# Kernel tuning notes

Measured on AMD Instinct MI355X. Metric: run time of the kernel, lower is better.

## Reference

```python
import jax, jax.numpy as jnp
import numpy as np

NEG_INF = -1e9


def setup_inputs() -> dict:
    key = jax.random.key(0)
    ks = jax.random.split(key, 12)
    B, Tq, Tki, E, D, M = 4, 2048, 2048, 1024, 128, 16384
    return {
        "x": jax.random.normal(ks[0], (B, Tq, E), jnp.float32),
        "ki": jax.random.normal(ks[1], (B, Tki, E), jnp.float32),
        "vi": jax.random.normal(ks[2], (B, Tki, E), jnp.float32),
        "mem_keys": jax.random.normal(ks[3], (B, M, D), jnp.float32),
        "mem_vals": jax.random.normal(ks[4], (B, M, D), jnp.float32),
        "Wq": jax.random.normal(ks[5], (E, D), jnp.float32) / np.sqrt(E),
        "bq": jax.random.normal(ks[6], (D,), jnp.float32) * 0.02,
        "Wk": jax.random.normal(ks[7], (E, D), jnp.float32) / np.sqrt(E),
        "bk": jax.random.normal(ks[8], (D,), jnp.float32) * 0.02,
        "Wv": jax.random.normal(ks[9], (E, D), jnp.float32) / np.sqrt(E),
        "bv": jax.random.normal(ks[10], (D,), jnp.float32) * 0.02,
        "gate": jax.random.normal(ks[11], (1,), jnp.float32),
        "idx": 3,
    }


def reference(x, ki, vi, mem_keys, mem_vals, Wq, bq, Wk, bk, Wv, bv, gate, idx):
    B, Tq, E = x.shape
    D = Wq.shape[1]
    top_k = 32
    q = x @ Wq + bq            # [B,Tq,D]
    k = x @ Wk + bk            # [B,Tq,D]
    v = x @ Wv + bv
    s = idx * D                # idx is a python int -> static slice
    k_full = jnp.concatenate([ki[:, :, s:s + D], k], axis=1)   # [B,Tk,D]
    v_full = jnp.concatenate([vi[:, :, s:s + D], v], axis=1)
    Tk = k_full.shape[1]
    # causal SDPA over prefix+current, offset diagonal Tk-Tq
    scores = jnp.einsum("bqd,bkd->bqk", q, k_full) / jnp.sqrt(jnp.float32(D))
    i = jnp.arange(Tq)[:, None]
    j = jnp.arange(Tk)[None, :]
    causal = j <= i + (Tk - Tq)
    scores = jnp.where(causal, scores, NEG_INF)
    att = jax.nn.softmax(scores, axis=-1)
    out = jnp.einsum("bqk,bkd->bqd", att, v_full)              # [B,Tq,D]
    # kNN memory attention: exact top-k inner-product search per query
    mem_scores = jnp.einsum("btd,bmd->btm", q, mem_keys)       # [B,Tq,M]
    _, top_idx = jax.lax.top_k(mem_scores, top_k)              # [B,Tq,K]
    gather = jax.vmap(lambda mem, ix: mem[ix])                 # per batch
    mem_k = gather(mem_keys, top_idx)                          # [B,Tq,K,D]
    mem_v = gather(mem_vals, top_idx)
    # note: original scales by sqrt(Cq)=sqrt(n_embd), not sqrt(head_size)
    mem_att = jax.nn.softmax(
        jnp.einsum("btd,btkd->btk", q, mem_k) / jnp.sqrt(jnp.float32(E)), axis=-1)
    mem_out = jnp.einsum("btk,btkd->btd", mem_att, mem_v)      # [B,Tq,D]
    md_out = out * gate + mem_out * (1.0 - gate)
    return md_out
```

## Files before the change

### kernel.cpp

```cpp
#include <hip/hip_runtime.h>


using bf16x8 = __attribute__((ext_vector_type(8))) short;
using f32x4  = __attribute__((ext_vector_type(4))) float;

typedef __attribute__((address_space(1))) const void GVoid;
typedef __attribute__((address_space(3))) void LVoid;
__device__ __forceinline__ void gl16(const ushort* g, ushort* l) {
  __builtin_amdgcn_global_load_lds((GVoid*)g, (LVoid*)l, 16, 0, 0);
}

__device__ __forceinline__ float bf2f(ushort h) {
  union { uint u; float f; } x; x.u = ((uint)h) << 16; return x.f;
}
__device__ __forceinline__ ushort f2bf(float f) {
  union { float f; uint u; } x; x.f = f;
  uint u = x.u;
  u += 0x7fffu + ((u >> 16) & 1u);
  return (ushort)(u >> 16);
}
__device__ __forceinline__ uint ord2(uint v) {
  uint s = (v >> 15) & 0x00010001u;
  uint t = (s << 15) - s;
  return v ^ t ^ 0x80008000u;
}

__global__ __launch_bounds__(256) void k_wt(const float* __restrict__ Wq,
                                            const float* __restrict__ Wk,
                                            const float* __restrict__ Wv,
                                            ushort* __restrict__ Wth,
                                            ushort* __restrict__ Wtlq) {
  int id = blockIdx.x * 256 + threadIdx.x;
  int z = id >> 17, r = id & 131071;
  int n = r >> 10, k = r & 1023;
  const float* W = (z == 1) ? Wk : (z == 2) ? Wv : Wq;
  float w = W[k * 128 + n];
  ushort h = f2bf(w);
  if (z < 3) Wth[id] = h;
  else       Wtlq[r] = f2bf(w - bf2f(h));
}

__global__ __launch_bounds__(256) void k_cvt8(const float* __restrict__ src,
                                              ushort* __restrict__ dst) {
  int id = blockIdx.x * 256 + threadIdx.x;
  size_t base = (size_t)id * 8;
  float4 a = *(const float4*)(src + base);
  float4 b = *(const float4*)(src + base + 4);
  bf16x8 r;
  r[0] = (short)f2bf(a.x); r[1] = (short)f2bf(a.y);
  r[2] = (short)f2bf(a.z); r[3] = (short)f2bf(a.w);
  r[4] = (short)f2bf(b.x); r[5] = (short)f2bf(b.y);
  r[6] = (short)f2bf(b.z); r[7] = (short)f2bf(b.w);
  *(bf16x8*)(dst + base) = r;
}

__global__ __launch_bounds__(256) void k_xsplit(const float* __restrict__ x,
                                                ushort* __restrict__ xh,
                                                ushort* __restrict__ xl) {
  int id = blockIdx.x * 256 + threadIdx.x;
  size_t base = (size_t)id * 8;
  float4 a = *(const float4*)(x + base);
  float4 b = *(const float4*)(x + base + 4);
  float xf[8] = {a.x, a.y, a.z, a.w, b.x, b.y, b.z, b.w};
  bf16x8 rh, rl;
#pragma unroll
  for (int j = 0; j < 8; ++j) {
    ushort h = f2bf(xf[j]);
    rh[j] = (short)h;
    rl[j] = (short)f2bf(xf[j] - bf2f(h));
  }
  *(bf16x8*)(xh + base) = rh;
  *(bf16x8*)(xl + base) = rl;
}

__global__ __launch_bounds__(256) void k_prefix(const float* __restrict__ ki,
                                                const float* __restrict__ vi,
                                                const int* __restrict__ idx,
                                                ushort* __restrict__ kfull,
                                                ushort* __restrict__ vfull) {
  int s = idx[0] * 128;
  int id = blockIdx.x * 256 + threadIdx.x;
  int d8 = (id & 15) * 8;
  int bt = id >> 4;
  int b = bt >> 11, t = bt & 2047;
  const float* kp = ki + (size_t)bt * 1024 + s + d8;
  const float* vp = vi + (size_t)bt * 1024 + s + d8;
  bf16x8 rk, rv;
#pragma unroll
  for (int j = 0; j < 8; ++j) { rk[j] = (short)f2bf(kp[j]); rv[j] = (short)f2bf(vp[j]); }
  size_t dst = ((size_t)b * 4096 + t) * 128 + d8;
  *(bf16x8*)(kfull + dst) = rk;
  *(bf16x8*)(vfull + dst) = rv;
}

__global__ __launch_bounds__(256) void k_qkv3(const ushort* __restrict__ xh,
                                              const ushort* __restrict__ xl,
                                              const ushort* __restrict__ Wth,
                                              const ushort* __restrict__ Wtlq,
                                              const float* __restrict__ bq,
                                              const float* __restrict__ bk,
                                              const float* __restrict__ bv,
                                              float* __restrict__ qex,
                                              ushort* __restrict__ kfull,
                                              ushort* __restrict__ vfull) {
  __shared__ ushort lds[2][16384];
  int z = blockIdx.z;
  int g = blockIdx.y;
  int m0 = blockIdx.x * 64;
  int tid = threadIdx.x;
  int w = tid >> 6, lane = tid & 63;
  int l15 = lane & 15, q8 = (lane >> 4) * 8;
  const ushort* Wz = Wth + (size_t)z * 131072;
  const ushort* xh_src = xh + (size_t)(m0 + w * 16 + l15) * 1024 + q8;
  const ushort* xl_src = xl + (size_t)(m0 + w * 16 + l15) * 1024 + q8;
  const ushort* wh_src = Wz   + (size_t)(g * 64 + w * 16 + l15) * 1024 + q8;
  const ushort* wl_src = Wtlq + (size_t)(g * 64 + w * 16 + l15) * 1024 + q8;
  int sb = w * 1024;

  f32x4 zero = {0.f, 0.f, 0.f, 0.f};
  f32x4 acc[4] = {zero, zero, zero, zero};

  {
    ushort* B = &lds[0][0];
    gl16(xh_src,      B + sb);
    gl16(xh_src + 32, B + sb + 512);
    gl16(wh_src,      B + 8192 + sb);
    gl16(wh_src + 32, B + 8192 + sb + 512);
    if (z == 0) {
      gl16(xl_src,      B + 4096 + sb);
      gl16(xl_src + 32, B + 4096 + sb + 512);
      gl16(wl_src,      B + 12288 + sb);
      gl16(wl_src + 32, B + 12288 + sb + 512);
    }
  }
  __syncthreads();
  int bf = 0;
  for (int t16 = 0; t16 < 16; ++t16) {
    if (t16 < 15) {
      int k0 = t16 * 64 + 64;
      ushort* B = &lds[bf ^ 1][0];
      gl16(xh_src + k0,      B + sb);
      gl16(xh_src + k0 + 32, B + sb + 512);
      gl16(wh_src + k0,      B + 8192 + sb);
      gl16(wh_src + k0 + 32, B + 8192 + sb + 512);
      if (z == 0) {
        gl16(xl_src + k0,      B + 4096 + sb);
        gl16(xl_src + k0 + 32, B + 4096 + sb + 512);
        gl16(wl_src + k0,      B + 12288 + sb);
        gl16(wl_src + k0 + 32, B + 12288 + sb + 512);
      }
    }
    const ushort* B = &lds[bf][0];
    int lo = lane * 8;
    if (z == 0) {
#pragma unroll
      for (int kc = 0; kc < 2; ++kc) {
        bf16x8 ah = *(const bf16x8*)(B + (w * 2 + kc) * 512 + lo);
        bf16x8 al = *(const bf16x8*)(B + 4096 + (w * 2 + kc) * 512 + lo);
#pragma unroll
        for (int cc = 0; cc < 4; ++cc) {
          bf16x8 bh = *(const bf16x8*)(B + 8192 + (cc * 2 + kc) * 512 + lo);
          bf16x8 bl = *(const bf16x8*)(B + 12288 + (cc * 2 + kc) * 512 + lo);
          acc[cc] = __builtin_amdgcn_mfma_f32_16x16x32_bf16(ah, bh, acc[cc], 0, 0, 0);
          acc[cc] = __builtin_amdgcn_mfma_f32_16x16x32_bf16(ah, bl, acc[cc], 0, 0, 0);
          acc[cc] = __builtin_amdgcn_mfma_f32_16x16x32_bf16(al, bh, acc[cc], 0, 0, 0);
        }
      }
    } else {
#pragma unroll
      for (int kc = 0; kc < 2; ++kc) {
        bf16x8 ah = *(const bf16x8*)(B + (w * 2 + kc) * 512 + lo);
#pragma unroll
        for (int cc = 0; cc < 4; ++cc) {
          bf16x8 bh = *(const bf16x8*)(B + 8192 + (cc * 2 + kc) * 512 + lo);
          acc[cc] = __builtin_amdgcn_mfma_f32_16x16x32_bf16(ah, bh, acc[cc], 0, 0, 0);
        }
      }
    }
    __syncthreads();
    bf ^= 1;
  }

  const float* bias = (z == 0) ? bq : (z == 1) ? bk : bv;
  int mrow = m0 + w * 16 + (lane >> 4) * 4;
#pragma unroll
  for (int cc = 0; cc < 4; ++cc) {
    int n = g * 64 + cc * 16 + l15;
    float bb = bias[n];
#pragma unroll
    for (int r = 0; r < 4; ++r) {
      int m = mrow + r;
      float val = acc[cc][r] + bb;
      if (z == 0) {
        qex[(size_t)m * 128 + n] = val;
      } else {
        int b2 = m >> 11, tt = m & 2047;
        size_t o = ((size_t)b2 * 4096 + 2048 + tt) * 128 + n;
        if (z == 1) kfull[o] = f2bf(val); else vfull[o] = f2bf(val);
      }
    }
  }
}

__global__ __launch_bounds__(256) void k_vt(const ushort* __restrict__ vfull,
                                            ushort* __restrict__ Vt) {
  __shared__ ushort lds[64][136];
  int blk = blockIdx.x;
  int b = blk >> 6, t0 = (blk & 63) * 64;
  int t = threadIdx.x;
#pragma unroll
  for (int p = 0; p < 4; ++p) {
    int ch = p * 256 + t;
    int row = ch >> 4, c8 = (ch & 15) * 8;
    uint4 v = *(const uint4*)(vfull + ((size_t)b * 4096 + t0 + row) * 128 + c8);
    *(uint4*)(&lds[row][c8]) = v;
  }
  __syncthreads();
#pragma unroll
  for (int p = 0; p < 8; ++p) {
    int q = p * 256 + t;
    int d = q >> 4, t4 = (q & 15) * 4;
    ushort4 o;
    o.x = lds[t4 + 0][d]; o.y = lds[t4 + 1][d];
    o.z = lds[t4 + 2][d]; o.w = lds[t4 + 3][d];
    *(ushort4*)(Vt + ((size_t)b * 128 + d) * 4096 + t0 + t4) = o;
  }
}

__global__ __launch_bounds__(256) void k_scores(const float* __restrict__ A,
                                                const ushort* __restrict__ Bm,
                                                ushort* __restrict__ S,
                                                int N, int nslice, int causalOff,
                                                long sA, long sB, long sS) {
  __shared__ ushort Bt[64 * 136];
  int q0 = blockIdx.x * 64;
  int ns0 = blockIdx.y * nslice;
  int nend = ns0 + nslice; if (nend > N) nend = N;
  int climit = q0 + 64 + causalOff; if (nend > climit) nend = climit;
  if (ns0 >= nend) return;
  int zb = blockIdx.z;
  const float*  Ab = A  + (size_t)zb * sA;
  const ushort* Bb = Bm + (size_t)zb * sB;
  ushort* Sb = S + (size_t)zb * sS;
  int t = threadIdx.x, lane = t & 63, wv = t >> 6;
  int l15 = lane & 15, q8 = (lane >> 4) * 8;
  const float* Arow = Ab + (size_t)(q0 + wv * 16 + l15) * 128 + q8;
  bf16x8 af[4];
#pragma unroll
  for (int kc = 0; kc < 4; ++kc)
#pragma unroll
    for (int j = 0; j < 8; ++j) af[kc][j] = (short)f2bf(Arow[kc * 32 + j]);
  for (int n0 = ns0; n0 < nend; n0 += 64) {
#pragma unroll
    for (int p = 0; p < 4; ++p) {
      int ch = p * 256 + t;
      int row = ch >> 4, c8 = (ch & 15) * 8;
      uint4 v = *(const uint4*)(Bb + (size_t)(n0 + row) * 128 + c8);
      *(uint4*)(&Bt[row * 136 + c8]) = v;
    }
    __syncthreads();
    f32x4 zero = {0.f, 0.f, 0.f, 0.f};
    f32x4 acc[4] = {zero, zero, zero, zero};
#pragma unroll
    for (int h = 0; h < 4; ++h) {
#pragma unroll
      for (int kc = 0; kc < 4; ++kc) {
        bf16x8 bfr = *(const bf16x8*)(&Bt[(h * 16 + l15) * 136 + kc * 32 + q8]);
        acc[h] = __builtin_amdgcn_mfma_f32_16x16x32_bf16(af[kc], bfr, acc[h], 0, 0, 0);
      }
    }
    int qq = q0 + wv * 16 + (lane >> 4) * 4;
#pragma unroll
    for (int h = 0; h < 4; ++h)
#pragma unroll
      for (int r = 0; r < 4; ++r)
        Sb[(size_t)(qq + r) * N + (n0 + h * 16 + l15)] = f2bf(acc[h][r]);
    __syncthreads();
  }
}

__global__ __launch_bounds__(256) void k_softmax(ushort* __restrict__ S) {
  int rid = blockIdx.x;
  int i = rid & 2047;
  ushort* row = S + (size_t)rid * 4096;
  int w = i + 2049;
  int t = threadIdx.x;
  const float scale = 0.08838834764831845f;
  float v[16];
  float mx = -1e30f;
#pragma unroll
  for (int c = 0; c < 16; ++c) {
    int e = c * 256 + t;
    float f = -1e30f;
    if (e < w) f = bf2f(row[e]) * scale;
    v[c] = f;
    mx = fmaxf(mx, f);
  }
  __shared__ float red[4];
#pragma unroll
  for (int off = 32; off; off >>= 1) mx = fmaxf(mx, __shfl_xor(mx, off));
  if ((t & 63) == 0) red[t >> 6] = mx;
  __syncthreads();
  mx = fmaxf(fmaxf(red[0], red[1]), fmaxf(red[2], red[3]));
  __syncthreads();
  float ex[16];
  float sum = 0.f;
#pragma unroll
  for (int c = 0; c < 16; ++c) {
    int e = c * 256 + t;
    ex[c] = (e < w) ? __expf(v[c] - mx) : 0.f;
    sum += ex[c];
  }
#pragma unroll
  for (int off = 32; off; off >>= 1) sum += __shfl_xor(sum, off);
  if ((t & 63) == 0) red[t >> 6] = sum;
  __syncthreads();
  sum = red[0] + red[1] + red[2] + red[3];
  float inv = 1.f / sum;
#pragma unroll
  for (int c = 0; c < 16; ++c) {
    int e = c * 256 + t;
    row[e] = f2bf(ex[c] * inv);
  }
}

__global__ __launch_bounds__(128) void k_pv(const ushort* __restrict__ P,
                                            const ushort* __restrict__ Vt,
                                            float* __restrict__ O) {
  __shared__ ushort lds[2][4096];
  int b = blockIdx.z;
  int d0 = blockIdx.y * 32;
  int q0 = blockIdx.x * 32;
  int t = threadIdx.x, lane = t & 63, w = t >> 6;
  int l15 = lane & 15, q8 = (lane >> 4) * 8;
  const ushort* Pq = P + ((size_t)b * 2048 + q0) * 4096;
  const ushort* Vb = Vt + (size_t)b * 128 * 4096;
  const ushort* p_src = Pq + (size_t)(w * 16 + l15) * 4096 + q8;
  const ushort* v_src = Vb + (size_t)(d0 + w * 16 + l15) * 4096 + q8;
  int kend = q0 + 32 + 2048; if (kend > 4096) kend = 4096;
  int ksteps = (kend + 63) >> 6;

  f32x4 zero = {0.f, 0.f, 0.f, 0.f};
  f32x4 acc[2] = {zero, zero};

  {
    ushort* B = &lds[0][0];
    gl16(p_src,      B + (w * 2 + 0) * 512);
    gl16(p_src + 32, B + (w * 2 + 1) * 512);
    gl16(v_src,      B + 2048 + (w * 2 + 0) * 512);
    gl16(v_src + 32, B + 2048 + (w * 2 + 1) * 512);
  }
  __syncthreads();
  int bf = 0;
  for (int st = 0; st < ksteps; ++st) {
    if (st + 1 < ksteps) {
      int k0 = st * 64 + 64;
      ushort* B = &lds[bf ^ 1][0];
      gl16(p_src + k0,      B + (w * 2 + 0) * 512);
      gl16(p_src + k0 + 32, B + (w * 2 + 1) * 512);
      gl16(v_src + k0,      B + 2048 + (w * 2 + 0) * 512);
      gl16(v_src + k0 + 32, B + 2048 + (w * 2 + 1) * 512);
    }
    const ushort* B = &lds[bf][0];
    int lo = lane * 8;
#pragma unroll
    for (int kc = 0; kc < 2; ++kc) {
      bf16x8 af = *(const bf16x8*)(B + (w * 2 + kc) * 512 + lo);
#pragma unroll
      for (int nc = 0; nc < 2; ++nc) {
        bf16x8 bfr = *(const bf16x8*)(B + 2048 + (nc * 2 + kc) * 512 + lo);
        acc[nc] = __builtin_amdgcn_mfma_f32_16x16x32_bf16(af, bfr, acc[nc], 0, 0, 0);
      }
    }
    __syncthreads();
    bf ^= 1;
  }

  size_t ob = ((size_t)b * 2048 + q0 + w * 16 + (lane >> 4) * 4) * 128;
#pragma unroll
  for (int nc = 0; nc < 2; ++nc)
#pragma unroll
    for (int r = 0; r < 4; ++r)
      O[ob + (size_t)r * 128 + d0 + nc * 16 + l15] = acc[nc][r];
}

__global__ __launch_bounds__(256) void k_topk(const ushort* __restrict__ Sall,
                                              const float* __restrict__ qf32b,
                                              const float* __restrict__ memk,
                                              const float* __restrict__ memv,
                                              float* __restrict__ mout) {
  __shared__ uint sred[32];
  __shared__ float qf[128];
  __shared__ uint cidx[384];
  __shared__ float csc[384];
  __shared__ unsigned long long ckey[384];
  __shared__ uint selIdx[32];
  __shared__ float selS[32];
  __shared__ float obuf[256];
  __shared__ int nC;

  int i = blockIdx.x;
  const ushort* Srow = Sall + (size_t)i * 16384;
  int t = threadIdx.x;
  int wv = t >> 6, lane = t & 63;
  if (t < 128) qf[t] = qf32b[(size_t)i * 128 + t];
  if (t == 0) nC = 0;

  uint keys[32];
#pragma unroll
  for (int c = 0; c < 8; ++c) {
    int base = (c * 256 + t) * 8;
    uint4 rv = *(const uint4*)(Srow + base);
    keys[c * 4 + 0] = ord2(rv.x);
    keys[c * 4 + 1] = ord2(rv.y);
    keys[c * 4 + 2] = ord2(rv.z);
    keys[c * 4 + 3] = ord2(rv.w);
  }
  uint mymax = 0;
#pragma unroll
  for (int r = 0; r < 32; ++r) {
    uint v = keys[r];
    uint hi = v >> 16, lo = v & 0xffffu;
    uint mm = hi > lo ? hi : lo;
    mymax = mm > mymax ? mm : mymax;
  }
#pragma unroll
  for (int off = 32; off; off >>= 1) {
    uint o = __shfl_xor(mymax, off);
    mymax = o > mymax ? o : mymax;
  }
  if (lane == 0) sred[wv] = mymax;
  __syncthreads();
  uint M = sred[0];
  { uint a = sred[1]; M = a > M ? a : M;
    a = sred[2]; M = a > M ? a : M;
    a = sred[3]; M = a > M ? a : M; }
  __syncthreads();

  uint T;
  uint MbCur = M >> 5;
  uint carry = 0;
  while (true) {
    uint h0 = 0, h1 = 0;
#pragma unroll
    for (int r = 0; r < 32; ++r) {
      uint v = keys[r];
      uint blo = MbCur - ((v & 0xffffu) >> 5);
      uint bhi = MbCur - (v >> 21);
      if (blo < 8u) { uint a = 1u << ((blo & 3u) << 3); if (blo < 4u) h0 += a; else h1 += a; }
      if (bhi < 8u) { uint a = 1u << ((bhi & 3u) << 3); if (bhi < 4u) h0 += a; else h1 += a; }
    }
    uint c8[8] = {h0 & 255u, (h0 >> 8) & 255u, (h0 >> 16) & 255u, h0 >> 24,
                  h1 & 255u, (h1 >> 8) & 255u, (h1 >> 16) & 255u, h1 >> 24};
#pragma unroll
    for (int b = 0; b < 8; ++b)
#pragma unroll
      for (int off = 32; off; off >>= 1) c8[b] += __shfl_xor(c8[b], off);
    if (lane == 0) {
#pragma unroll
      for (int b = 0; b < 8; ++b) sred[wv * 8 + b] = c8[b];
    }
    __syncthreads();
    uint cum = carry; int bstar = -1;
#pragma unroll
    for (int b = 0; b < 8; ++b) {
      uint tb = sred[b] + sred[8 + b] + sred[16 + b] + sred[24 + b];
      cum += tb;
      if (bstar < 0 && cum >= 64u) bstar = b;
    }
    if (bstar >= 0) { T = (MbCur - (uint)bstar) << 5; break; }
    carry = cum;
    MbCur -= 8u;
    __syncthreads();
  }

#pragma unroll
  for (int r = 0; r < 32; ++r) {
    uint v = keys[r];
    int base = ((r >> 2) * 256 + t) * 8 + ((r & 3) * 2);
    if ((v & 0xffffu) >= T) { int p = atomicAdd(&nC, 1); if (p < 384) cidx[p] = (uint)base; }
    if ((v >> 16) >= T)     { int p = atomicAdd(&nC, 1); if (p < 384) cidx[p] = (uint)(base + 1); }
  }
  __syncthreads();
  int C = nC; if (C > 384) C = 384;
  {
    float qa = qf[lane * 2], qb = qf[lane * 2 + 1];
    for (int j0 = wv; j0 < C; j0 += 32) {
      float2 pp[8];
      float s[8];
#pragma unroll
      for (int u = 0; u < 8; ++u) {
        int j = j0 + u * 4;
        if (j < C) pp[u] = *(const float2*)(memk + (size_t)cidx[j] * 128 + lane * 2);
      }
#pragma unroll
      for (int u = 0; u < 8; ++u) {
        int j = j0 + u * 4;
        s[u] = (j < C) ? (qa * pp[u].x + qb * pp[u].y) : 0.f;
      }
#pragma unroll
      for (int off = 32; off; off >>= 1) {
#pragma unroll
        for (int u = 0; u < 8; ++u) s[u] += __shfl_xor(s[u], off);
      }
      if (lane == 0) {
#pragma unroll
        for (int u = 0; u < 8; ++u) {
          int j = j0 + u * 4;
          if (j < C) csc[j] = s[u];
        }
      }
    }
  }
  __syncthreads();
  for (int j = t; j < C; j += 256) {
    uint sb2 = __float_as_uint(csc[j]);
    uint o = (sb2 & 0x80000000u) ? ~sb2 : (sb2 | 0x80000000u);
    ckey[j] = ((unsigned long long)o << 32) | (uint)(~cidx[j]);
  }
  __syncthreads();
  for (int j = t; j < C; j += 256) {
    unsigned long long my = ckey[j];
    int rank = 0;
    for (int l = 0; l < C; ++l) rank += (ckey[l] > my) ? 1 : 0;
    if (rank < 32) { selS[rank] = csc[j]; selIdx[rank] = cidx[j]; }
  }
  __syncthreads();
  if (wv == 0) {
    float sc = (lane < 32) ? selS[lane] * 0.03125f : -1e30f;
    float mx = sc;
#pragma unroll
    for (int off = 32; off; off >>= 1) mx = fmaxf(mx, __shfl_xor(mx, off));
    float ex = (lane < 32) ? __expf(sc - mx) : 0.f;
    float Z = ex;
#pragma unroll
    for (int off = 32; off; off >>= 1) Z += __shfl_xor(Z, off);
    if (lane < 32) selS[lane] = ex / Z;
  }
  __syncthreads();
  {
    int d = t & 127, half = t >> 7;
    float vv[16];
#pragma unroll
    for (int u = 0; u < 16; ++u)
      vv[u] = memv[(size_t)selIdx[half * 16 + u] * 128 + d];
    float acc = 0.f;
#pragma unroll
    for (int u = 0; u < 16; ++u)
      acc += selS[half * 16 + u] * vv[u];
    obuf[t] = acc;
  }
  __syncthreads();
  if (t < 128) mout[(size_t)i * 128 + t] = obuf[t] + obuf[t + 128];
}

__global__ __launch_bounds__(256) void k_mix(const float* __restrict__ a,
                                             const float* __restrict__ b,
                                             const float* __restrict__ gate,
                                             float* __restrict__ out) {
  int id = blockIdx.x * 256 + threadIdx.x;
  float g = gate[0];
  float4 va = ((const float4*)a)[id];
  float4 vb = ((const float4*)b)[id];
  float4 o;
  o.x = va.x * g + vb.x * (1.f - g);
  o.y = va.y * g + vb.y * (1.f - g);
  o.z = va.z * g + vb.z * (1.f - g);
  o.w = va.w * g + vb.w * (1.f - g);
  ((float4*)out)[id] = o;
}

extern "C" void kernel_launch(void* const* d_in, const int* in_sizes, int n_in,
                              void* d_out, int out_size, void* d_ws, size_t ws_size,
                              hipStream_t stream) {
  const float* x    = (const float*)d_in[0];
  const float* ki   = (const float*)d_in[1];
  const float* vi   = (const float*)d_in[2];
  const float* mk   = (const float*)d_in[3];
  const float* mv   = (const float*)d_in[4];
  const float* Wq   = (const float*)d_in[5];
  const float* bq   = (const float*)d_in[6];
  const float* Wk   = (const float*)d_in[7];
  const float* bk   = (const float*)d_in[8];
  const float* Wv   = (const float*)d_in[9];
  const float* bv   = (const float*)d_in[10];
  const float* gate = (const float*)d_in[11];
  const int*   idx  = (const int*)d_in[12];

  char* ws = (char*)d_ws;
  ushort* Sbuf  = (ushort*)(ws);
  ushort* xh    = (ushort*)(ws);
  ushort* xl    = (ushort*)(ws + 16777216);
  float*  qex   = (float*) (ws + 67108864);
  ushort* kfull = (ushort*)(ws + 71303168);
  ushort* vfull = (ushort*)(ws + 75497472);
  ushort* Vt    = (ushort*)(ws + 79691776);
  ushort* mkb   = (ushort*)(ws + 83886080);
  ushort* Wth   = (ushort*)(ws + 100663296);
  ushort* Wtlq  = (ushort*)(ws + 101449728);
  float*  osdpa = (float*) (ws + 101711872);
  float*  mout  = (float*) (ws + 105906176);

  k_wt<<<2048, 256, 0, stream>>>(Wq, Wk, Wv, Wth, Wtlq);
  k_cvt8<<<4096, 256, 0, stream>>>(mk, mkb);
  k_xsplit<<<4096, 256, 0, stream>>>(x, xh, xl);
  k_prefix<<<512, 256, 0, stream>>>(ki, vi, idx, kfull, vfull);

  k_qkv3<<<dim3(128, 2, 3), 256, 0, stream>>>(xh, xl, Wth, Wtlq, bq, bk, bv,
                                              qex, kfull, vfull);
  k_vt<<<256, 256, 0, stream>>>(vfull, Vt);

  k_scores<<<dim3(32, 8, 4), 256, 0, stream>>>(qex, kfull, Sbuf,
                                               4096, 512, 2048,
                                               (long)2048 * 128, (long)4096 * 128,
                                               (long)2048 * 4096);
  k_softmax<<<8192, 256, 0, stream>>>(Sbuf);
  k_pv<<<dim3(64, 4, 4), 128, 0, stream>>>(Sbuf, Vt, osdpa);

  for (int b = 0; b < 4; ++b) {
    k_scores<<<dim3(32, 32, 1), 256, 0, stream>>>(qex + (size_t)b * 2048 * 128,
                                                  mkb + (size_t)b * 16384 * 128,
                                                  Sbuf, 16384, 512, (1 << 28),
                                                  0, 0, 0);
    k_topk<<<2048, 256, 0, stream>>>(Sbuf, qex + (size_t)b * 2048 * 128,
                                     mk + (size_t)b * 16384 * 128,
                                     mv + (size_t)b * 16384 * 128,
                                     mout + (size_t)b * 2048 * 128);
  }

  k_mix<<<1024, 256, 0, stream>>>(osdpa, mout, gate, (float*)d_out);
}
```

Measured before the change: 690.3 us.

## Overlap next-batch memory scores with current-batch top-k via fused double-buffered kernel

Adds a combined kernel whose first 1024 blocks compute the memory-score GEMM for batch b+1 into one buffer, while the remaining blocks run top-k and gather for batch b from the other buffer. Shared memory is carved out of one common byte array so both roles fit in a single launch. The aim is to fill the idle compute that the memory-bound top-k leaves, and to cut launch count, by running it alongside the MFMA-heavy scoring. It needs a larger workspace for a second 64MB score buffer and falls back to the old serial loop when the workspace is too small. Mixing two kinds of blocks in one launch may also change occupancy and scheduling.

```diff
diff --git a/kernel.cpp b/kernel.cpp
--- a/kernel.cpp
+++ b/kernel.cpp
@@ -227,56 +227,65 @@
   }
 }
 
+__device__ __forceinline__ void scores_body(ushort* Bt,
+                                            const float* A, const ushort* Bm,
+                                            ushort* S, int N, int nslice,
+                                            int causalOff, long sA, long sB,
+                                            long sS, int bx, int by, int bz,
+                                            int t) {
+  int q0 = bx * 64;
+  int ns0 = by * nslice;
+  int nend = ns0 + nslice; if (nend > N) nend = N;
+  int climit = q0 + 64 + causalOff; if (nend > climit) nend = climit;
+  if (ns0 >= nend) return;
+  const float*  Ab = A  + (size_t)bz * sA;
+  const ushort* Bb = Bm + (size_t)bz * sB;
+  ushort* Sb = S + (size_t)bz * sS;
+  int lane = t & 63, wv = t >> 6;
+  int l15 = lane & 15, q8 = (lane >> 4) * 8;
+  const float* Arow = Ab + (size_t)(q0 + wv * 16 + l15) * 128 + q8;
+  bf16x8 af[4];
+#pragma unroll
+  for (int kc = 0; kc < 4; ++kc)
+#pragma unroll
+    for (int j = 0; j < 8; ++j) af[kc][j] = (short)f2bf(Arow[kc * 32 + j]);
+  for (int n0 = ns0; n0 < nend; n0 += 64) {
+#pragma unroll
+    for (int p = 0; p < 4; ++p) {
+      int ch = p * 256 + t;
+      int row = ch >> 4, c8 = (ch & 15) * 8;
+      uint4 v = *(const uint4*)(Bb + (size_t)(n0 + row) * 128 + c8);
+      *(uint4*)(&Bt[row * 136 + c8]) = v;
+    }
+    __syncthreads();
+    f32x4 zero = {0.f, 0.f, 0.f, 0.f};
+    f32x4 acc[4] = {zero, zero, zero, zero};
+#pragma unroll
+    for (int h = 0; h < 4; ++h) {
+#pragma unroll
+      for (int kc = 0; kc < 4; ++kc) {
+        bf16x8 bfr = *(const bf16x8*)(&Bt[(h * 16 + l15) * 136 + kc * 32 + q8]);
+        acc[h] = __builtin_amdgcn_mfma_f32_16x16x32_bf16(af[kc], bfr, acc[h], 0, 0, 0);
+      }
+    }
+    int qq = q0 + wv * 16 + (lane >> 4) * 4;
+#pragma unroll
+    for (int h = 0; h < 4; ++h)
+#pragma unroll
+      for (int r = 0; r < 4; ++r)
+        Sb[(size_t)(qq + r) * N + (n0 + h * 16 + l15)] = f2bf(acc[h][r]);
+    __syncthreads();
+  }
+}
+
 __global__ __launch_bounds__(256) void k_scores(const float* __restrict__ A,
                                                 const ushort* __restrict__ Bm,
                                                 ushort* __restrict__ S,
                                                 int N, int nslice, int causalOff,
                                                 long sA, long sB, long sS) {
-  __shared__ ushort Bt[64 * 136];
-  int q0 = blockIdx.x * 64;
-  int ns0 = blockIdx.y * nslice;
-  int nend = ns0 + nslice; if (nend > N) nend = N;
-  int climit = q0 + 64 + causalOff; if (nend > climit) nend = climit;
-  if (ns0 >= nend) return;
-  int zb = blockIdx.z;
-  const float*  Ab = A  + (size_t)zb * sA;
-  const ushort* Bb = Bm + (size_t)zb * sB;
-  ushort* Sb = S + (size_t)zb * sS;
-  int t = threadIdx.x, lane = t & 63, wv = t >> 6;
-  int l15 = lane & 15, q8 = (lane >> 4) * 8;
-  const float* Arow = Ab + (size_t)(q0 + wv * 16 + l15) * 128 + q8;
-  bf16x8 af[4];
-#pragma unroll
-  for (int kc = 0; kc < 4; ++kc)
-#pragma unroll
-    for (int j = 0; j < 8; ++j) af[kc][j] = (short)f2bf(Arow[kc * 32 + j]);
-  for (int n0 = ns0; n0 < nend; n0 += 64) {
-#pragma unroll
-    for (int p = 0; p < 4; ++p) {
-      int ch = p * 256 + t;
-      int row = ch >> 4, c8 = (ch & 15) * 8;
-      uint4 v = *(const uint4*)(Bb + (size_t)(n0 + row) * 128 + c8);
-      *(uint4*)(&Bt[row * 136 + c8]) = v;
-    }
-    __syncthreads();
-    f32x4 zero = {0.f, 0.f, 0.f, 0.f};
-    f32x4 acc[4] = {zero, zero, zero, zero};
-#pragma unroll
-    for (int h = 0; h < 4; ++h) {
-#pragma unroll
-      for (int kc = 0; kc < 4; ++kc) {
-        bf16x8 bfr = *(const bf16x8*)(&Bt[(h * 16 + l15) * 136 + kc * 32 + q8]);
-        acc[h] = __builtin_amdgcn_mfma_f32_16x16x32_bf16(af[kc], bfr, acc[h], 0, 0, 0);
-      }
-    }
-    int qq = q0 + wv * 16 + (lane >> 4) * 4;
-#pragma unroll
-    for (int h = 0; h < 4; ++h)
-#pragma unroll
-      for (int r = 0; r < 4; ++r)
-        Sb[(size_t)(qq + r) * N + (n0 + h * 16 + l15)] = f2bf(acc[h][r]);
-    __syncthreads();
-  }
+  __shared__ __align__(16) ushort Bt[64 * 136];
+  scores_body(Bt, A, Bm, S, N, nslice, causalOff, sA, sB, sS,
+              blockIdx.x, blockIdx.y, blockIdx.z, threadIdx.x);
 }
 
 __global__ __launch_bounds__(256) void k_softmax(ushort* __restrict__ S) {
@@ -384,24 +393,23 @@
       O[ob + (size_t)r * 128 + d0 + nc * 16 + l15] = acc[nc][r];
 }
 
-__global__ __launch_bounds__(256) void k_topk(const ushort* __restrict__ Sall,
-                                              const float* __restrict__ qf32b,
-                                              const float* __restrict__ memk,
-                                              const float* __restrict__ memv,
-                                              float* __restrict__ mout) {
+__device__ __forceinline__ void topk_body(char* smem,
+                                          const ushort* Sall,
+                                          const float* qf32b,
+                                          const float* memk,
+                                          const float* memv,
+                                          float* mout, int i, int t) {
+  unsigned long long* ckey = (unsigned long long*)smem;
+  float* csc  = (float*)(smem + 3072);
+  uint*  cidx = (uint*)(smem + 4608);
+  float* qf   = (float*)(smem + 6144);
+  float* obuf = (float*)(smem + 6656);
   __shared__ uint sred[32];
-  __shared__ float qf[128];
-  __shared__ uint cidx[384];
-  __shared__ float csc[384];
-  __shared__ unsigned long long ckey[384];
   __shared__ uint selIdx[32];
   __shared__ float selS[32];
-  __shared__ float obuf[256];
   __shared__ int nC;
 
-  int i = blockIdx.x;
   const ushort* Srow = Sall + (size_t)i * 16384;
-  int t = threadIdx.x;
   int wv = t >> 6, lane = t & 63;
   if (t < 128) qf[t] = qf32b[(size_t)i * 128 + t];
   if (t == 0) nC = 0;
@@ -552,6 +560,34 @@
   }
   __syncthreads();
   if (t < 128) mout[(size_t)i * 128 + t] = obuf[t] + obuf[t + 128];
+}
+
+__global__ __launch_bounds__(256) void k_topk(const ushort* __restrict__ Sall,
+                                              const float* __restrict__ qf32b,
+                                              const float* __restrict__ memk,
+                                              const float* __restrict__ memv,
+                                              float* __restrict__ mout) {
+  __shared__ __align__(16) char smem[7680];
+  topk_body(smem, Sall, qf32b, memk, memv, mout, blockIdx.x, threadIdx.x);
+}
+
+__global__ __launch_bounds__(256) void k_both(const ushort* __restrict__ Sall,
+                                              const float* __restrict__ qf32b,
+                                              const float* __restrict__ memk,
+                                              const float* __restrict__ memv,
+                                              float* __restrict__ mout,
+                                              const float* __restrict__ A2,
+                                              const ushort* __restrict__ Bm2,
+                                              ushort* __restrict__ S2) {
+  __shared__ __align__(16) char smem[64 * 136 * 2];
+  if (blockIdx.x < 1024) {
+    int bx = blockIdx.x;
+    scores_body((ushort*)smem, A2, Bm2, S2, 16384, 512, (1 << 28),
+                0, 0, 0, bx & 31, bx >> 5, 0, threadIdx.x);
+  } else {
+    topk_body(smem, Sall, qf32b, memk, memv, mout,
+              blockIdx.x - 1024, threadIdx.x);
+  }
 }
 
 __global__ __launch_bounds__(256) void k_mix(const float* __restrict__ a,
@@ -588,18 +624,40 @@
   const int*   idx  = (const int*)d_in[12];
 
   char* ws = (char*)d_ws;
-  ushort* Sbuf  = (ushort*)(ws);
-  ushort* xh    = (ushort*)(ws);
-  ushort* xl    = (ushort*)(ws + 16777216);
-  float*  qex   = (float*) (ws + 67108864);
-  ushort* kfull = (ushort*)(ws + 71303168);
-  ushort* vfull = (ushort*)(ws + 75497472);
-  ushort* Vt    = (ushort*)(ws + 79691776);
-  ushort* mkb   = (ushort*)(ws + 83886080);
-  ushort* Wth   = (ushort*)(ws + 100663296);
-  ushort* Wtlq  = (ushort*)(ws + 101449728);
-  float*  osdpa = (float*) (ws + 101711872);
-  float*  mout  = (float*) (ws + 105906176);
+  const size_t NEED_OVL = 177209344ull;
+  bool ovl = (ws_size >= NEED_OVL);
+
+  ushort *S_A, *S_B, *xh, *xl, *kfull, *vfull, *Vt, *mkb, *Wth, *Wtlq;
+  float *qex, *osdpa, *mout;
+  if (ovl) {
+    S_A   = (ushort*)(ws);
+    xh    = (ushort*)(ws);
+    xl    = (ushort*)(ws + 16777216);
+    S_B   = (ushort*)(ws + 67108864);
+    qex   = (float*) (ws + 134217728);
+    kfull = (ushort*)(ws + 138412032);
+    vfull = (ushort*)(ws + 142606336);
+    Vt    = (ushort*)(ws + 146800640);
+    mkb   = (ushort*)(ws + 150994944);
+    Wth   = (ushort*)(ws + 167772160);
+    Wtlq  = (ushort*)(ws + 168558592);
+    osdpa = (float*) (ws + 168820736);
+    mout  = (float*) (ws + 173015040);
+  } else {
+    S_A   = (ushort*)(ws);
+    S_B   = S_A;
+    xh    = (ushort*)(ws);
+    xl    = (ushort*)(ws + 16777216);
+    qex   = (float*) (ws + 67108864);
+    kfull = (ushort*)(ws + 71303168);
+    vfull = (ushort*)(ws + 75497472);
+    Vt    = (ushort*)(ws + 79691776);
+    mkb   = (ushort*)(ws + 83886080);
+    Wth   = (ushort*)(ws + 100663296);
+    Wtlq  = (ushort*)(ws + 101449728);
+    osdpa = (float*) (ws + 101711872);
+    mout  = (float*) (ws + 105906176);
+  }
 
   k_wt<<<2048, 256, 0, stream>>>(Wq, Wk, Wv, Wth, Wtlq);
   k_cvt8<<<4096, 256, 0, stream>>>(mk, mkb);
@@ -610,22 +668,46 @@
                                               qex, kfull, vfull);
   k_vt<<<256, 256, 0, stream>>>(vfull, Vt);
 
-  k_scores<<<dim3(32, 8, 4), 256, 0, stream>>>(qex, kfull, Sbuf,
+  k_scores<<<dim3(32, 8, 4), 256, 0, stream>>>(qex, kfull, S_A,
                                                4096, 512, 2048,
                                                (long)2048 * 128, (long)4096 * 128,
                                                (long)2048 * 4096);
-  k_softmax<<<8192, 256, 0, stream>>>(Sbuf);
-  k_pv<<<dim3(64, 4, 4), 128, 0, stream>>>(Sbuf, Vt, osdpa);
-
-  for (int b = 0; b < 4; ++b) {
-    k_scores<<<dim3(32, 32, 1), 256, 0, stream>>>(qex + (size_t)b * 2048 * 128,
-                                                  mkb + (size_t)b * 16384 * 128,
-                                                  Sbuf, 16384, 512, (1 << 28),
+  k_softmax<<<8192, 256, 0, stream>>>(S_A);
+  k_pv<<<dim3(64, 4, 4), 128, 0, stream>>>(S_A, Vt, osdpa);
+
+  if (ovl) {
+    k_scores<<<dim3(32, 32, 1), 256, 0, stream>>>(qex, mkb, S_B,
+                                                  16384, 512, (1 << 28),
                                                   0, 0, 0);
-    k_topk<<<2048, 256, 0, stream>>>(Sbuf, qex + (size_t)b * 2048 * 128,
-                                     mk + (size_t)b * 16384 * 128,
-                                     mv + (size_t)b * 16384 * 128,
-                                     mout + (size_t)b * 2048 * 128);
+    ushort* Scur = S_B;
+    ushort* Snxt = S_A;
+    for (int b = 0; b < 3; ++b) {
+      k_both<<<3072, 256, 0, stream>>>(Scur,
+                                       qex + (size_t)b * 2048 * 128,
+                                       mk + (size_t)b * 16384 * 128,
+                                       mv + (size_t)b * 16384 * 128,
+                                       mout + (size_t)b * 2048 * 128,
+                                       qex + (size_t)(b + 1) * 2048 * 128,
+                                       mkb + (size_t)(b + 1) * 16384 * 128,
+                                       Snxt);
+      ushort* tmp = Scur; Scur = Snxt; Snxt = tmp;
+    }
+    k_topk<<<2048, 256, 0, stream>>>(Scur,
+                                     qex + (size_t)3 * 2048 * 128,
+                                     mk + (size_t)3 * 16384 * 128,
+                                     mv + (size_t)3 * 16384 * 128,
+                                     mout + (size_t)3 * 2048 * 128);
+  } else {
+    for (int b = 0; b < 4; ++b) {
+      k_scores<<<dim3(32, 32, 1), 256, 0, stream>>>(qex + (size_t)b * 2048 * 128,
+                                                    mkb + (size_t)b * 16384 * 128,
+                                                    S_A, 16384, 512, (1 << 28),
+                                                    0, 0, 0);
+      k_topk<<<2048, 256, 0, stream>>>(S_A, qex + (size_t)b * 2048 * 128,
+                                       mk + (size_t)b * 16384 * 128,
+                                       mv + (size_t)b * 16384 * 128,
+                                       mout + (size_t)b * 2048 * 128);
+    }
   }
 
   k_mix<<<1024, 256, 0, stream>>>(osdpa, mout, gate, (float*)d_out);
```

After: 746.2 us. +8.1%, slower.

## Prune top-k candidates using per-chunk score maxima emitted by score GEMM

Applied to the files above, without the earlier changes.

The memory score GEMM now also writes the max score of each 64-column chunk per query row. The top-k kernel ranks the 256 chunk maxima, takes the 64th largest as a threshold, and scans only chunks whose max reaches it, instead of loading the whole 16384-score row and running an iterative histogram search. This cuts global reads and ALU work in top-k, at the cost of a small extra reduction and store in the GEMM epilogue and a 256x256 rank loop in shared memory. Candidate selection still keeps every score at or above the threshold, and the 384-entry candidate cap stays as before.

```diff
diff --git a/kernel.cpp b/kernel.cpp
--- a/kernel.cpp
+++ b/kernel.cpp
@@ -23,6 +23,10 @@
   uint s = (v >> 15) & 0x00010001u;
   uint t = (s << 15) - s;
   return v ^ t ^ 0x80008000u;
+}
+__device__ __forceinline__ ushort ord1(ushort h) {
+  uint s = (h >> 15) & 1u;
+  return (ushort)(h ^ ((s << 15) - s) ^ 0x8000u);
 }
 
 __global__ __launch_bounds__(256) void k_wt(const float* __restrict__ Wq,
@@ -230,6 +234,7 @@
 __global__ __launch_bounds__(256) void k_scores(const float* __restrict__ A,
                                                 const ushort* __restrict__ Bm,
                                                 ushort* __restrict__ S,
+                                                ushort* __restrict__ cmax,
                                                 int N, int nslice, int causalOff,
                                                 long sA, long sB, long sS) {
   __shared__ ushort Bt[64 * 136];
@@ -275,6 +280,16 @@
 #pragma unroll
       for (int r = 0; r < 4; ++r)
         Sb[(size_t)(qq + r) * N + (n0 + h * 16 + l15)] = f2bf(acc[h][r]);
+    if (cmax) {
+#pragma unroll
+      for (int r = 0; r < 4; ++r) {
+        float m = fmaxf(fmaxf(acc[0][r], acc[1][r]), fmaxf(acc[2][r], acc[3][r]));
+#pragma unroll
+        for (int off = 1; off < 16; off <<= 1) m = fmaxf(m, __shfl_xor(m, off));
+        if (l15 == 0)
+          cmax[(size_t)(qq + r) * 256 + (n0 >> 6)] = ord1(f2bf(m));
+      }
+    }
     __syncthreads();
   }
 }
@@ -385,11 +400,13 @@
 }
 
 __global__ __launch_bounds__(256) void k_topk(const ushort* __restrict__ Sall,
+                                              const ushort* __restrict__ cmaxA,
                                               const float* __restrict__ qf32b,
                                               const float* __restrict__ memk,
                                               const float* __restrict__ memv,
                                               float* __restrict__ mout) {
-  __shared__ uint sred[32];
+  __shared__ ushort marr[256];
+  __shared__ ushort chun[256];
   __shared__ float qf[128];
   __shared__ uint cidx[384];
   __shared__ float csc[384];
@@ -397,92 +414,50 @@
   __shared__ uint selIdx[32];
   __shared__ float selS[32];
   __shared__ float obuf[256];
-  __shared__ int nC;
+  __shared__ int nF, nC;
+  __shared__ uint sT;
 
   int i = blockIdx.x;
   const ushort* Srow = Sall + (size_t)i * 16384;
   int t = threadIdx.x;
   int wv = t >> 6, lane = t & 63;
   if (t < 128) qf[t] = qf32b[(size_t)i * 128 + t];
-  if (t == 0) nC = 0;
-
-  uint keys[32];
-#pragma unroll
-  for (int c = 0; c < 8; ++c) {
-    int base = (c * 256 + t) * 8;
+  if (t == 0) { nF = 0; nC = 0; }
+  uint cm = cmaxA[(size_t)i * 256 + t];
+  marr[t] = (ushort)cm;
+  __syncthreads();
+
+  {
+    int rank = 0;
+#pragma unroll 8
+    for (int j = 0; j < 256; ++j) {
+      uint vj = marr[j];
+      rank += (vj > cm) || (vj == cm && j < t);
+    }
+    if (rank == 63) sT = cm;
+  }
+  __syncthreads();
+  uint T = sT;
+  if (cm >= T) { int p = atomicAdd(&nF, 1); chun[p] = (ushort)t; }
+  __syncthreads();
+  int F = nF;
+
+  for (int jj = (t >> 3); jj < F; jj += 32) {
+    int base = ((int)chun[jj]) * 64 + (t & 7) * 8;
     uint4 rv = *(const uint4*)(Srow + base);
-    keys[c * 4 + 0] = ord2(rv.x);
-    keys[c * 4 + 1] = ord2(rv.y);
-    keys[c * 4 + 2] = ord2(rv.z);
-    keys[c * 4 + 3] = ord2(rv.w);
-  }
-  uint mymax = 0;
-#pragma unroll
-  for (int r = 0; r < 32; ++r) {
-    uint v = keys[r];
-    uint hi = v >> 16, lo = v & 0xffffu;
-    uint mm = hi > lo ? hi : lo;
-    mymax = mm > mymax ? mm : mymax;
-  }
-#pragma unroll
-  for (int off = 32; off; off >>= 1) {
-    uint o = __shfl_xor(mymax, off);
-    mymax = o > mymax ? o : mymax;
-  }
-  if (lane == 0) sred[wv] = mymax;
-  __syncthreads();
-  uint M = sred[0];
-  { uint a = sred[1]; M = a > M ? a : M;
-    a = sred[2]; M = a > M ? a : M;
-    a = sred[3]; M = a > M ? a : M; }
-  __syncthreads();
-
-  uint T;
-  uint MbCur = M >> 5;
-  uint carry = 0;
-  while (true) {
-    uint h0 = 0, h1 = 0;
-#pragma unroll
-    for (int r = 0; r < 32; ++r) {
-      uint v = keys[r];
-      uint blo = MbCur - ((v & 0xffffu) >> 5);
-      uint bhi = MbCur - (v >> 21);
-      if (blo < 8u) { uint a = 1u << ((blo & 3u) << 3); if (blo < 4u) h0 += a; else h1 += a; }
-      if (bhi < 8u) { uint a = 1u << ((bhi & 3u) << 3); if (bhi < 4u) h0 += a; else h1 += a; }
-    }
-    uint c8[8] = {h0 & 255u, (h0 >> 8) & 255u, (h0 >> 16) & 255u, h0 >> 24,
-                  h1 & 255u, (h1 >> 8) & 255u, (h1 >> 16) & 255u, h1 >> 24};
-#pragma unroll
-    for (int b = 0; b < 8; ++b)
-#pragma unroll
-      for (int off = 32; off; off >>= 1) c8[b] += __shfl_xor(c8[b], off);
-    if (lane == 0) {
-#pragma unroll
-      for (int b = 0; b < 8; ++b) sred[wv * 8 + b] = c8[b];
-    }
-    __syncthreads();
-    uint cum = carry; int bstar = -1;
-#pragma unroll
-    for (int b = 0; b < 8; ++b) {
-      uint tb = sred[b] + sred[8 + b] + sred[16 + b] + sred[24 + b];
-      cum += tb;
-      if (bstar < 0 && cum >= 64u) bstar = b;
-    }
-    if (bstar >= 0) { T = (MbCur - (uint)bstar) << 5; break; }
-    carry = cum;
-    MbCur -= 8u;
-    __syncthreads();
-  }
-
-#pragma unroll
-  for (int r = 0; r < 32; ++r) {
-    uint v = keys[r];
-    int base = ((r >> 2) * 256 + t) * 8 + ((r & 3) * 2);
-    if ((v & 0xffffu) >= T) { int p = atomicAdd(&nC, 1); if (p < 384) cidx[p] = (uint)base; }
-    if ((v >> 16) >= T)     { int p = atomicAdd(&nC, 1); if (p < 384) cidx[p] = (uint)(base + 1); }
+    uint a0 = ord2(rv.x), a1 = ord2(rv.y), a2 = ord2(rv.z), a3 = ord2(rv.w);
+    if ((a0 & 0xffffu) >= T) { int p = atomicAdd(&nC, 1); if (p < 384) cidx[p] = (uint)(base + 0); }
+    if ((a0 >> 16)     >= T) { int p = atomicAdd(&nC, 1); if (p < 384) cidx[p] = (uint)(base + 1); }
+    if ((a1 & 0xffffu) >= T) { int p = atomicAdd(&nC, 1); if (p < 384) cidx[p] = (uint)(base + 2); }
+    if ((a1 >> 16)     >= T) { int p = atomicAdd(&nC, 1); if (p < 384) cidx[p] = (uint)(base + 3); }
+    if ((a2 & 0xffffu) >= T) { int p = atomicAdd(&nC, 1); if (p < 384) cidx[p] = (uint)(base + 4); }
+    if ((a2 >> 16)     >= T) { int p = atomicAdd(&nC, 1); if (p < 384) cidx[p] = (uint)(base + 5); }
+    if ((a3 & 0xffffu) >= T) { int p = atomicAdd(&nC, 1); if (p < 384) cidx[p] = (uint)(base + 6); }
+    if ((a3 >> 16)     >= T) { int p = atomicAdd(&nC, 1); if (p < 384) cidx[p] = (uint)(base + 7); }
   }
   __syncthreads();
   int C = nC; if (C > 384) C = 384;
+
   {
     float qa = qf[lane * 2], qb = qf[lane * 2 + 1];
     for (int j0 = wv; j0 < C; j0 += 32) {
@@ -600,6 +575,7 @@
   ushort* Wtlq  = (ushort*)(ws + 101449728);
   float*  osdpa = (float*) (ws + 101711872);
   float*  mout  = (float*) (ws + 105906176);
+  ushort* cmaxb = (ushort*)(ws + 110100480);
 
   k_wt<<<2048, 256, 0, stream>>>(Wq, Wk, Wv, Wth, Wtlq);
   k_cvt8<<<4096, 256, 0, stream>>>(mk, mkb);
@@ -610,7 +586,7 @@
                                               qex, kfull, vfull);
   k_vt<<<256, 256, 0, stream>>>(vfull, Vt);
 
-  k_scores<<<dim3(32, 8, 4), 256, 0, stream>>>(qex, kfull, Sbuf,
+  k_scores<<<dim3(32, 8, 4), 256, 0, stream>>>(qex, kfull, Sbuf, nullptr,
                                                4096, 512, 2048,
                                                (long)2048 * 128, (long)4096 * 128,
                                                (long)2048 * 4096);
@@ -620,9 +596,11 @@
   for (int b = 0; b < 4; ++b) {
     k_scores<<<dim3(32, 32, 1), 256, 0, stream>>>(qex + (size_t)b * 2048 * 128,
                                                   mkb + (size_t)b * 16384 * 128,
-                                                  Sbuf, 16384, 512, (1 << 28),
+                                                  Sbuf, cmaxb,
+                                                  16384, 512, (1 << 28),
                                                   0, 0, 0);
-    k_topk<<<2048, 256, 0, stream>>>(Sbuf, qex + (size_t)b * 2048 * 128,
+    k_topk<<<2048, 256, 0, stream>>>(Sbuf, cmaxb,
+                                     qex + (size_t)b * 2048 * 128,
                                      mk + (size_t)b * 16384 * 128,
                                      mv + (size_t)b * 16384 * 128,
                                      mout + (size_t)b * 2048 * 128);
```

Result: faster. 611.2 us (-11.5%).
